# Optimization experiments

Hardware: AMD Instinct MI355X
Metric: run time of the kernel (lower is better)

Reference implementation:

```python
import jax, jax.numpy as jnp
import numpy as np

B, S, H = 2, 2048, 4096
NH, NKV, HD = 32, 8, 128
THETA = 1000000.0
NEG = jnp.finfo(jnp.float32).min


def setup_inputs() -> dict:
    key = jax.random.key(0)
    ks = jax.random.split(key, 9)
    s = 0.02
    return {
        "hidden_states": jax.random.normal(ks[0], (B, S, H), jnp.float32),
        "position_ids": jnp.tile(jnp.arange(S, dtype=jnp.int32)[None, :], (B, 1)),
        "Wq": jax.random.normal(ks[1], (NH * HD, H), jnp.float32) * s,
        "bq": jax.random.normal(ks[2], (NH * HD,), jnp.float32) * s,
        "Wk": jax.random.normal(ks[3], (NKV * HD, H), jnp.float32) * s,
        "bk": jax.random.normal(ks[4], (NKV * HD,), jnp.float32) * s,
        "Wv": jax.random.normal(ks[5], (NKV * HD, H), jnp.float32) * s,
        "bv": jax.random.normal(ks[6], (NKV * HD,), jnp.float32) * s,
        "Wo": jax.random.normal(ks[7], (H, H), jnp.float32) * s,
        "bo": jax.random.normal(ks[8], (H,), jnp.float32) * s,
    }


def _rotate_half_interleaved(x):
    # y[..., ::2] = -x[..., 1::2]; y[..., 1::2] = x[..., ::2]
    x2 = x.reshape(*x.shape[:-1], -1, 2)
    y = jnp.stack([-x2[..., 1], x2[..., 0]], axis=-1)
    return y.reshape(x.shape)


def reference(hidden_states, position_ids, Wq, bq, Wk, bk, Wv, bv, Wo, bo):
    bsz, q_len, _ = hidden_states.shape
    q = (hidden_states @ Wq.T + bq).reshape(bsz, q_len, NH, HD).transpose(0, 2, 1, 3)
    k = (hidden_states @ Wk.T + bk).reshape(bsz, q_len, NKV, HD).transpose(0, 2, 1, 3)
    v = (hidden_states @ Wv.T + bv).reshape(bsz, q_len, NKV, HD).transpose(0, 2, 1, 3)

    # rotary embedding (interleaved / repeat_interleave variant)
    inv_freq = 1.0 / (THETA ** (jnp.arange(0, HD, 2, dtype=jnp.float32) / HD))
    freqs = position_ids.astype(jnp.float32)[:, :, None] * inv_freq[None, None, :]  # [B,S,HD/2]
    emb = jnp.repeat(freqs, 2, axis=-1)  # [B,S,HD]
    cos = jnp.cos(emb)[:, None, :, :]  # [B,1,S,HD]
    sin = jnp.sin(emb)[:, None, :, :]
    q = q * cos + _rotate_half_interleaved(q) * sin
    k = k * cos + _rotate_half_interleaved(k) * sin

    # GQA: repeat KV heads (repeat_interleave on head axis)
    n_rep = NH // NKV
    k = jnp.repeat(k, n_rep, axis=1)
    v = jnp.repeat(v, n_rep, axis=1)

    scores = jnp.einsum("bhqd,bhkd->bhqk", q, k) / np.sqrt(HD).astype(np.float32)
    causal = jnp.tril(jnp.ones((q_len, q_len), dtype=bool))
    scores = jnp.where(causal[None, None, :, :], scores, NEG)
    attn = jax.nn.softmax(scores.astype(jnp.float32), axis=-1).astype(q.dtype)
    out = jnp.einsum("bhqk,bhkd->bhqd", attn, v)
    out = out.transpose(0, 2, 1, 3).reshape(bsz, q_len, H)
    return out @ Wo.T + bo
```

## Files before the change

kernel.cpp:

```cpp
#include <hip/hip_runtime.h>
#include <stdint.h>

typedef __bf16 bf16x8 __attribute__((ext_vector_type(8)));
typedef float f32x4 __attribute__((ext_vector_type(4)));
typedef float f32x16 __attribute__((ext_vector_type(16)));

#define S_LEN 2048
#define NKVH 8
#define HDIM 128
#define MROWS 4096
#define LDQKV 6144
#define SCALE 0.08838834764831845f
#define C_LOG2 0.1275405707067851f
#define THR_RAW 62.7f

__device__ __forceinline__ unsigned short f2bf(float f) {
  unsigned u = __float_as_uint(f);
  u += 0x7FFFu + ((u >> 16) & 1u);
  return (unsigned short)(u >> 16);
}
__device__ __forceinline__ float bf2f(unsigned short h) {
  return __uint_as_float(((unsigned)h) << 16);
}

__device__ __forceinline__ void gload16(const unsigned short* g, unsigned short* l) {
  __builtin_amdgcn_global_load_lds(
      (__attribute__((address_space(1))) void*)(g),
      (__attribute__((address_space(3))) void*)(l), 16, 0, 0);
}

__global__ void cast_f32_bf16(const float4* __restrict__ in, ushort4* __restrict__ out, int n4) {
  int i = blockIdx.x * 256 + threadIdx.x;
  const int stride = gridDim.x * 256;
  for (; i < n4; i += stride) {
    float4 v = in[i];
    ushort4 o;
    o.x = f2bf(v.x); o.y = f2bf(v.y); o.z = f2bf(v.z); o.w = f2bf(v.w);
    out[i] = o;
  }
}

template <int OUTF>
__global__ __launch_bounds__(512, 2)
void gemm256(const unsigned short* __restrict__ A,
             const unsigned short* __restrict__ Bw,
             const float* __restrict__ bias,
             void* __restrict__ C,
             int ldc, int K) {
  __shared__ unsigned short lds[2][4][8192];

  const int t = threadIdx.x;
  const int lane = t & 63;
  const int w = t >> 6;
  const int wr = w >> 2, wc = w & 3;
  const int row16 = lane & 15, kgrp = lane >> 4;
  const int m0 = blockIdx.y * 256, n0 = blockIdx.x * 256;

  const int riu = t >> 3;
  const int col = (((t & 7) ^ (riu & 7)) << 3);
  const int rB0 = (riu & 31) + ((riu >> 5) << 6);
  const unsigned short* pA = A + (size_t)(m0 + riu) * K + col;
  const unsigned short* pB = Bw + (size_t)(n0 + rB0) * K + col;

#define STG(nb_, u_, src_)                                                  \
  {                                                                         \
    gload16((src_), &lds[nb_][u_][t * 8]);                                  \
    gload16((src_) + (size_t)128 * K, &lds[nb_][u_][4096 + t * 8]);         \
  }

  const int sw = row16 & 7;
  const int abase = (wr * 64 + row16) * 64;
  const int bbase = (wc * 32 + row16) * 64;

  f32x4 acc[8][4];
#pragma unroll
  for (int i = 0; i < 8; i++)
#pragma unroll
    for (int j = 0; j < 4; j++) acc[i][j] = (f32x4){0.f, 0.f, 0.f, 0.f};

  bf16x8 afr[4][2], bfr[2][2][2];
  const int NT = K >> 6;

  STG(0, 0, pA);
  STG(0, 1, pB);
  STG(0, 2, pB + (size_t)32 * K);
  STG(0, 3, pA + (size_t)64 * K);

  for (int T = 0; T < NT; ++T) {
    const int cb = T & 1, nb = cb ^ 1;
    const unsigned short* Lc = &lds[cb][0][0];
    const size_t kk = (size_t)(T + 1) << 6;
    const bool st = (T + 1 < NT);

    asm volatile("s_waitcnt vmcnt(4)\n\ts_barrier" ::: "memory");
    if (st) STG(nb, 0, pA + kk);
#pragma unroll
    for (int mi = 0; mi < 4; mi++)
#pragma unroll
      for (int ks = 0; ks < 2; ks++)
        afr[mi][ks] = *(const bf16x8*)(Lc + abase + mi * 1024 + ((((ks << 2) + kgrp) ^ sw) << 3));
#pragma unroll
    for (int nj = 0; nj < 2; nj++)
#pragma unroll
      for (int ks = 0; ks < 2; ks++)
        bfr[0][nj][ks] = *(const bf16x8*)(Lc + 8192 + bbase + nj * 1024 + ((((ks << 2) + kgrp) ^ sw) << 3));
    __builtin_amdgcn_s_setprio(1);
#pragma unroll
    for (int mi = 0; mi < 4; mi++)
#pragma unroll
      for (int nj = 0; nj < 2; nj++)
#pragma unroll
        for (int ks = 0; ks < 2; ks++)
          acc[mi][nj] = __builtin_amdgcn_mfma_f32_16x16x32_bf16(afr[mi][ks], bfr[0][nj][ks], acc[mi][nj], 0, 0, 0);
    __builtin_amdgcn_s_setprio(0);

    if (st) {
      asm volatile("s_waitcnt vmcnt(4)\n\ts_barrier" ::: "memory");
      STG(nb, 1, pB + kk);
    } else {
      asm volatile("s_waitcnt vmcnt(2)\n\ts_barrier" ::: "memory");
    }
#pragma unroll
    for (int nj = 0; nj < 2; nj++)
#pragma unroll
      for (int ks = 0; ks < 2; ks++)
        bfr[1][nj][ks] = *(const bf16x8*)(Lc + 16384 + bbase + nj * 1024 + ((((ks << 2) + kgrp) ^ sw) << 3));
    __builtin_amdgcn_s_setprio(1);
#pragma unroll
    for (int mi = 0; mi < 4; mi++)
#pragma unroll
      for (int nj = 0; nj < 2; nj++)
#pragma unroll
        for (int ks = 0; ks < 2; ks++)
          acc[mi][2 + nj] = __builtin_amdgcn_mfma_f32_16x16x32_bf16(afr[mi][ks], bfr[1][nj][ks], acc[mi][2 + nj], 0, 0, 0);
    __builtin_amdgcn_s_setprio(0);

    if (st) {
      asm volatile("s_waitcnt vmcnt(4)\n\ts_barrier" ::: "memory");
      STG(nb, 2, pB + (size_t)32 * K + kk);
    } else {
      asm volatile("s_waitcnt vmcnt(0)\n\ts_barrier" ::: "memory");
    }
#pragma unroll
    for (int mi = 0; mi < 4; mi++)
#pragma unroll
      for (int ks = 0; ks < 2; ks++)
        afr[mi][ks] = *(const bf16x8*)(Lc + 24576 + abase + mi * 1024 + ((((ks << 2) + kgrp) ^ sw) << 3));
    __builtin_amdgcn_s_setprio(1);
#pragma unroll
    for (int mi = 0; mi < 4; mi++)
#pragma unroll
      for (int nj = 0; nj < 2; nj++)
#pragma unroll
        for (int ks = 0; ks < 2; ks++)
          acc[4 + mi][2 + nj] = __builtin_amdgcn_mfma_f32_16x16x32_bf16(afr[mi][ks], bfr[1][nj][ks], acc[4 + mi][2 + nj], 0, 0, 0);
    __builtin_amdgcn_s_setprio(0);

    if (st) {
      asm volatile("s_waitcnt vmcnt(4)\n\ts_barrier" ::: "memory");
      STG(nb, 3, pA + (size_t)64 * K + kk);
    } else {
      asm volatile("s_barrier" ::: "memory");
    }
    __builtin_amdgcn_s_setprio(1);
#pragma unroll
    for (int mi = 0; mi < 4; mi++)
#pragma unroll
      for (int nj = 0; nj < 2; nj++)
#pragma unroll
        for (int ks = 0; ks < 2; ks++)
          acc[4 + mi][nj] = __builtin_amdgcn_mfma_f32_16x16x32_bf16(afr[mi][ks], bfr[0][nj][ks], acc[4 + mi][nj], 0, 0, 0);
    __builtin_amdgcn_s_setprio(0);
  }
#undef STG

#pragma unroll
  for (int MI = 0; MI < 8; MI++) {
#pragma unroll
    for (int NJ = 0; NJ < 4; NJ++) {
      const int gr = m0 + wr * 128 + MI * 16 + kgrp * 4;
      const int gc = n0 + wc * 64 + NJ * 16 + row16;
      const float bv = bias[gc];
#pragma unroll
      for (int jj = 0; jj < 4; jj++) {
        float v = acc[MI][NJ][jj] + bv;
        if (OUTF) ((float*)C)[(size_t)(gr + jj) * ldc + gc] = v;
        else ((unsigned short*)C)[(size_t)(gr + jj) * ldc + gc] = f2bf(v);
      }
    }
  }
}

template <int OUTF>
__global__ __launch_bounds__(512, 2)
void gemm128(const unsigned short* __restrict__ A,
             const unsigned short* __restrict__ Bw,
             const float* __restrict__ bias,
             void* __restrict__ C,
             int ldc, int K) {
  __shared__ unsigned short lds[3 * 24576];

  const int t = threadIdx.x;
  const int lane = t & 63;
  const int w = t >> 6;
  const int wr = w >> 2, wc = w & 3;
  const int row16 = lane & 15, kgrp = lane >> 4;
  const int m0 = blockIdx.y * 128, n0 = blockIdx.x * 256;

  const int riu = t >> 3;
  const int col = (((t & 7) ^ (riu & 7)) << 3);
  const unsigned short* pA = A + (size_t)(m0 + riu) * K + col;
  const unsigned short* pB = Bw + (size_t)(n0 + riu) * K + col;

#define STG6(bo_, kk_)                                                      \
  {                                                                         \
    gload16(pA + (kk_), &lds[(bo_) + t * 8]);                               \
    gload16(pA + (size_t)64 * K + (kk_), &lds[(bo_) + 4096 + t * 8]);       \
    gload16(pB + (kk_), &lds[(bo_) + 8192 + t * 8]);                        \
    gload16(pB + (size_t)64 * K + (kk_), &lds[(bo_) + 12288 + t * 8]);      \
    gload16(pB + (size_t)128 * K + (kk_), &lds[(bo_) + 16384 + t * 8]);     \
    gload16(pB + (size_t)192 * K + (kk_), &lds[(bo_) + 20480 + t * 8]);     \
  }

  const int sw = row16 & 7;
  const int abase = (wr * 64 + row16) * 64;
  const int bbase = 8192 + (wc * 64 + row16) * 64;

  f32x4 acc[4][4];
#pragma unroll
  for (int i = 0; i < 4; i++)
#pragma unroll
    for (int j = 0; j < 4; j++) acc[i][j] = (f32x4){0.f, 0.f, 0.f, 0.f};

  bf16x8 afr[4][2], bfr[4][2];
  const int NT = K >> 6;

  STG6(0, 0);
  STG6(24576, 64);

  int rbc = 0;
  int rbs = 2;
  for (int T = 0; T < NT; ++T) {
    if (T < NT - 1) { asm volatile("s_waitcnt vmcnt(6)\n\ts_barrier" ::: "memory"); }
    else            { asm volatile("s_waitcnt vmcnt(0)\n\ts_barrier" ::: "memory"); }
    if (T + 2 < NT) STG6(rbs * 24576, (size_t)(T + 2) << 6);
    const unsigned short* Lc = &lds[rbc * 24576];

#pragma unroll
    for (int mi = 0; mi < 4; mi++)
#pragma unroll
      for (int ks = 0; ks < 2; ks++)
        afr[mi][ks] = *(const bf16x8*)(Lc + abase + mi * 1024 + ((((ks << 2) + kgrp) ^ sw) << 3));
#pragma unroll
    for (int nj = 0; nj < 4; nj++)
#pragma unroll
      for (int ks = 0; ks < 2; ks++)
        bfr[nj][ks] = *(const bf16x8*)(Lc + bbase + nj * 1024 + ((((ks << 2) + kgrp) ^ sw) << 3));

    __builtin_amdgcn_s_setprio(1);
#pragma unroll
    for (int mi = 0; mi < 4; mi++)
#pragma unroll
      for (int nj = 0; nj < 4; nj++)
#pragma unroll
        for (int ks = 0; ks < 2; ks++)
          acc[mi][nj] = __builtin_amdgcn_mfma_f32_16x16x32_bf16(afr[mi][ks], bfr[nj][ks], acc[mi][nj], 0, 0, 0);
    __builtin_amdgcn_s_setprio(0);

    rbc++; if (rbc == 3) rbc = 0;
    rbs++; if (rbs == 3) rbs = 0;
  }
#undef STG6

#pragma unroll
  for (int MI = 0; MI < 4; MI++) {
#pragma unroll
    for (int NJ = 0; NJ < 4; NJ++) {
      const int gr = m0 + wr * 64 + MI * 16 + kgrp * 4;
      const int gc = n0 + wc * 64 + NJ * 16 + row16;
      const float bv = bias[gc];
#pragma unroll
      for (int jj = 0; jj < 4; jj++) {
        float v = acc[MI][NJ][jj] + bv;
        if (OUTF) ((float*)C)[(size_t)(gr + jj) * ldc + gc] = v;
        else ((unsigned short*)C)[(size_t)(gr + jj) * ldc + gc] = f2bf(v);
      }
    }
  }
}

__global__ void rope_kernel(unsigned short* __restrict__ X,
                            const int* __restrict__ pos_ids,
                            int ncols, int ld) {
  const int perrow = ncols >> 3;
  int idx = blockIdx.x * 256 + threadIdx.x;
  const int row = idx / perrow;
  const int c0 = (idx - row * perrow) << 3;
  const float pos = (float)pos_ids[row];
  unsigned short* p = X + (size_t)row * ld + c0;
  uint4 v = *(uint4*)p;
  unsigned short* e = (unsigned short*)&v;
  const int p0 = (c0 & 127) >> 1;
#pragma unroll
  for (int q = 0; q < 4; ++q) {
    const float inv = exp2f(-(float)(p0 + q) * (19.931568569324174f / 64.f));
    const float fr = pos * inv;
    float sn, cs;
    __sincosf(fr, &sn, &cs);
    const float xe = bf2f(e[2 * q]);
    const float xo = bf2f(e[2 * q + 1]);
    e[2 * q]     = f2bf(xe * cs - xo * sn);
    e[2 * q + 1] = f2bf(xo * cs + xe * sn);
  }
  *(uint4*)p = v;
}

__global__ void transpose_v(const unsigned short* __restrict__ V, int ldv,
                            unsigned short* __restrict__ Vt) {
  __shared__ unsigned short tile[32][40];
  const int t = threadIdx.x;
  const int n0 = blockIdx.x * 32;
  const int m0 = blockIdx.y * 32;
  const int r = t >> 3;
  const int c = (t & 7) << 2;
  const unsigned short* src = V + (size_t)(m0 + r) * ldv + n0 + c;
  ushort4 d = *(const ushort4*)src;
  tile[r][c] = d.x; tile[r][c + 1] = d.y; tile[r][c + 2] = d.z; tile[r][c + 3] = d.w;
  __syncthreads();
  const int b = m0 >> 11;
  unsigned short* dst = Vt + (size_t)(b * 1024 + n0 + r) * 2048 + (m0 & 2047) + c;
  ushort4 o;
  o.x = tile[c][r]; o.y = tile[c + 1][r]; o.z = tile[c + 2][r]; o.w = tile[c + 3][r];
  *(ushort4*)dst = o;
}

__global__ __launch_bounds__(512, 2)
void attn_kernel2(const unsigned short* __restrict__ QKV,
                  const unsigned short* __restrict__ Vt,
                  unsigned short* __restrict__ O) {
  __shared__ unsigned short sK[2][64 * 128];
  __shared__ unsigned short sV[2][128 * 64];

  const int t = threadIdx.x;
  const int lane = t & 63;
  const int w = t >> 6;
  const int l31 = lane & 31;
  const int hi = lane >> 5;
  const int bid = blockIdx.x;
  int qt, bh;
  if (bid < 256) { qt = 7 - (bid >> 6); bh = bid & 63; }
  else           { qt = (bid - 256) >> 6; bh = bid & 63; }
  const int b = bh >> 5, h = bh & 31;
  const int kh = h >> 2;
  const int q0 = qt * 256;
  const int qw = q0 + w * 32;
  const int qg = qw + l31;

  const int ntiles = (q0 + 256) >> 6;
  const int myTiles = (qw + 95) >> 6;

  const int krow0 = t >> 4;
  const int kslot = t & 15;
  const int vrow0 = t >> 3;
  const int vslot = t & 7;
  const unsigned short* Kp = QKV + (size_t)(b * S_LEN) * LDQKV + 4096 + kh * HDIM;
  const unsigned short* Vp = Vt + (size_t)(b * 1024 + kh * HDIM) * 2048;
  const int ksw = (kslot ^ (krow0 & 7)) << 3;
  const int vsw = (vslot ^ (vrow0 & 7)) << 3;
  const unsigned short* KpA = Kp + (size_t)krow0 * LDQKV + ksw;
  const unsigned short* KpB = Kp + (size_t)(krow0 + 32) * LDQKV + ksw;
  const unsigned short* VpA = Vp + (size_t)vrow0 * 2048 + vsw;
  const unsigned short* VpB = Vp + (size_t)(vrow0 + 64) * 2048 + vsw;

#define STAGE(bufi, kv0m)                                              \
  {                                                                    \
    gload16(KpA + (size_t)(kv0m)*LDQKV, &sK[bufi][t * 8]);             \
    gload16(KpB + (size_t)(kv0m)*LDQKV, &sK[bufi][4096 + t * 8]);      \
    gload16(VpA + (kv0m), &sV[bufi][t * 8]);                           \
    gload16(VpB + (kv0m), &sV[bufi][4096 + t * 8]);                    \
  }

  bf16x8 qf[8];
  {
    const unsigned short* qb = QKV + (size_t)(b * S_LEN + qw + l31) * LDQKV + h * HDIM + hi * 8;
#pragma unroll
    for (int kd = 0; kd < 8; kd++) qf[kd] = *(const bf16x8*)(qb + kd * 16);
  }

  f32x16 o[4];
#pragma unroll
  for (int nt = 0; nt < 4; nt++)
#pragma unroll
    for (int r = 0; r < 16; r++) o[nt][r] = 0.f;
  float m = -1e30f, lsum = 0.f;

  const int rw7 = (l31 & 7) << 4;
  const int kswz = (hi << 4) ^ rw7;
  const int kbase0 = l31 * 128;
  const int vbase = l31 * 64;

  STAGE(0, 0);
  int buf = 0;
  for (int it = 0; it < ntiles; ++it) {
    if (it + 1 < ntiles) {
      STAGE(buf ^ 1, (it + 1) << 6);
      asm volatile("s_waitcnt vmcnt(4)" ::: "memory");
    } else {
      asm volatile("s_waitcnt vmcnt(0)" ::: "memory");
    }
    __builtin_amdgcn_s_barrier();

    if (it < myTiles) {
      const unsigned short* sKc = &sK[buf][0];
      const unsigned short* sVc = &sV[buf][0];
      const int kv0 = it << 6;

      f32x16 st[2];
#pragma unroll
      for (int r = 0; r < 16; r++) { st[0][r] = 0.f; st[1][r] = 0.f; }
      __builtin_amdgcn_s_setprio(1);
#pragma unroll
      for (int kd = 0; kd < 8; kd++) {
        bf16x8 k0 = *(const bf16x8*)(sKc + kbase0 + (((kd << 5) ^ kswz) >> 1));
        bf16x8 k1 = *(const bf16x8*)(sKc + 4096 + kbase0 + (((kd << 5) ^ kswz) >> 1));
        st[0] = __builtin_amdgcn_mfma_f32_32x32x16_bf16(k0, qf[kd], st[0], 0, 0, 0);
        st[1] = __builtin_amdgcn_mfma_f32_32x32x16_bf16(k1, qf[kd], st[1], 0, 0, 0);
      }
      __builtin_amdgcn_s_setprio(0);

      if (it == myTiles - 1) {
#pragma unroll
        for (int s2 = 0; s2 < 2; s2++)
#pragma unroll
          for (int r = 0; r < 16; r++) {
            const int kvg = kv0 + s2 * 32 + (r & 3) + 8 * (r >> 2) + 4 * hi;
            if (kvg > qg) st[s2][r] = -1e30f;
          }
      }

      float mx[8];
#pragma unroll
      for (int r = 0; r < 8; r++)
        mx[r] = fmaxf(fmaxf(st[0][r], st[0][r + 8]), fmaxf(st[1][r], st[1][r + 8]));
#pragma unroll
      for (int d = 4; d >= 1; d >>= 1)
#pragma unroll
        for (int r = 0; r < d; r++) mx[r] = fmaxf(mx[r], mx[r + d]);
      float tmax = fmaxf(mx[0], __shfl_xor(mx[0], 32));

      if (!__all(tmax <= m + THR_RAW)) {
        const float mnew = fmaxf(m, tmax);
        const float corr = exp2f((m - mnew) * C_LOG2);
        lsum *= corr;
#pragma unroll
        for (int r = 0; r < 16; r++) {
          const int src = (r & 3) + 8 * (r >> 2) + 4 * hi;
          const float cr = __shfl(corr, src);
#pragma unroll
          for (int nt = 0; nt < 4; nt++) o[nt][r] *= cr;
        }
        m = mnew;
      }
      const float mC = m * C_LOG2;

#pragma unroll
      for (int s2 = 0; s2 < 2; s2++)
#pragma unroll
        for (int r = 0; r < 16; r++) st[s2][r] = exp2f(fmaf(st[s2][r], C_LOG2, -mC));
      float sm[8];
#pragma unroll
      for (int r = 0; r < 8; r++)
        sm[r] = (st[0][r] + st[0][r + 8]) + (st[1][r] + st[1][r + 8]);
#pragma unroll
      for (int d = 4; d >= 1; d >>= 1)
#pragma unroll
        for (int r = 0; r < d; r++) sm[r] += sm[r + d];
      float tsum = sm[0] + __shfl_xor(sm[0], 32);
      lsum += tsum;

      bf16x8 pa[4];
#pragma unroll
      for (int s2 = 0; s2 < 2; s2++) {
        unsigned pw[8];
#pragma unroll
        for (int i = 0; i < 8; i++)
          asm("v_cvt_pk_bf16_f32 %0, %1, %2" : "=v"(pw[i]) : "v"(st[s2][2 * i]), "v"(st[s2][2 * i + 1]));
        const unsigned x0 = (unsigned)__shfl_xor((int)pw[0], 32);
        const unsigned x1 = (unsigned)__shfl_xor((int)pw[1], 32);
        const unsigned x2 = (unsigned)__shfl_xor((int)pw[2], 32);
        const unsigned x3 = (unsigned)__shfl_xor((int)pw[3], 32);
        const unsigned x4 = (unsigned)__shfl_xor((int)pw[4], 32);
        const unsigned x5 = (unsigned)__shfl_xor((int)pw[5], 32);
        const unsigned x6 = (unsigned)__shfl_xor((int)pw[6], 32);
        const unsigned x7 = (unsigned)__shfl_xor((int)pw[7], 32);
        union { unsigned u[4]; bf16x8 v; } u0, u1;
        u0.u[0] = hi ? x2 : pw[0];
        u0.u[1] = hi ? x3 : pw[1];
        u0.u[2] = hi ? pw[2] : x0;
        u0.u[3] = hi ? pw[3] : x1;
        u1.u[0] = hi ? x6 : pw[4];
        u1.u[1] = hi ? x7 : pw[5];
        u1.u[2] = hi ? pw[6] : x4;
        u1.u[3] = hi ? pw[7] : x5;
        pa[2 * s2] = u0.v; pa[2 * s2 + 1] = u1.v;
      }

      __builtin_amdgcn_s_setprio(1);
#pragma unroll
      for (int nt = 0; nt < 4; nt++) {
        const unsigned short* vr = sVc + vbase + nt * 2048;
#pragma unroll
        for (int ks = 0; ks < 4; ks++) {
          bf16x8 vb = *(const bf16x8*)(vr + (((ks << 5) ^ kswz) >> 1));
          o[nt] = __builtin_amdgcn_mfma_f32_32x32x16_bf16(pa[ks], vb, o[nt], 0, 0, 0);
        }
      }
      __builtin_amdgcn_s_setprio(0);
    }

    asm volatile("" ::: "memory");
    __builtin_amdgcn_s_barrier();
    buf ^= 1;
  }

  const float linv = 1.0f / lsum;
#pragma unroll
  for (int r = 0; r < 16; r++) {
    const int qr = (r & 3) + 8 * (r >> 2) + 4 * hi;
    const float lr = __shfl(linv, qr);
    unsigned short* orow = O + (size_t)(b * S_LEN + qw + qr) * 4096 + h * HDIM + l31;
#pragma unroll
    for (int nt = 0; nt < 4; nt++) orow[nt * 32] = f2bf(o[nt][r] * lr);
  }
#undef STAGE
}

extern "C" void kernel_launch(void* const* d_in, const int* in_sizes, int n_in,
                              void* d_out, int out_size, void* d_ws, size_t ws_size,
                              hipStream_t stream) {
  const float* hs = (const float*)d_in[0];
  const int*  pos = (const int*)d_in[1];
  const float* Wq = (const float*)d_in[2];
  const float* bq = (const float*)d_in[3];
  const float* Wk = (const float*)d_in[4];
  const float* bk = (const float*)d_in[5];
  const float* Wv = (const float*)d_in[6];
  const float* bv = (const float*)d_in[7];
  const float* Wo = (const float*)d_in[8];
  const float* bo = (const float*)d_in[9];
  float* out = (float*)d_out;

  char* ws = (char*)d_ws;
  unsigned short* hbf  = (unsigned short*)(ws);
  unsigned short* Wbuf = (unsigned short*)(ws + 33554432);
  unsigned short* QKV  = (unsigned short*)(ws + 83886080);
  unsigned short* Vtb  = (unsigned short*)(ws + 134217728);
  float*          biasb= (float*)(ws + 142606336);

  cast_f32_bf16<<<2048, 256, 0, stream>>>((const float4*)hs, (ushort4*)hbf, 4194304);
  cast_f32_bf16<<<2048, 256, 0, stream>>>((const float4*)Wq, (ushort4*)Wbuf, 4194304);
  cast_f32_bf16<<<1024, 256, 0, stream>>>((const float4*)Wk, (ushort4*)(Wbuf + 16777216), 1048576);
  cast_f32_bf16<<<1024, 256, 0, stream>>>((const float4*)Wv, (ushort4*)(Wbuf + 20971520), 1048576);
  hipMemcpyAsync(biasb, bq, 4096 * 4, hipMemcpyDeviceToDevice, stream);
  hipMemcpyAsync(biasb + 4096, bk, 1024 * 4, hipMemcpyDeviceToDevice, stream);
  hipMemcpyAsync(biasb + 5120, bv, 1024 * 4, hipMemcpyDeviceToDevice, stream);

  gemm256<0><<<dim3(16, 16), 512, 0, stream>>>(hbf, Wbuf, biasb, QKV, LDQKV, 4096);
  gemm128<0><<<dim3(8, 32), 512, 0, stream>>>(hbf, Wbuf + 16777216, biasb + 4096, QKV + 4096, LDQKV, 4096);

  cast_f32_bf16<<<2048, 256, 0, stream>>>((const float4*)Wo, (ushort4*)Wbuf, 4194304);

  rope_kernel<<<8192, 256, 0, stream>>>(QKV, pos, 4096, LDQKV);
  rope_kernel<<<2048, 256, 0, stream>>>(QKV + 4096, pos, 1024, LDQKV);

  transpose_v<<<dim3(32, 128), 256, 0, stream>>>(QKV + 5120, LDQKV, Vtb);

  attn_kernel2<<<dim3(512), 512, 0, stream>>>(QKV, Vtb, hbf);

  gemm256<1><<<dim3(16, 16), 512, 0, stream>>>(hbf, Wbuf, bo, out, 4096, 4096);
}
```

Baseline: 528.8 us.

## Shrink attention blocks to 128 queries, single-buffer KV, raise occupancy

The attention kernel now uses 256-thread blocks covering 128 query rows instead of 512 threads covering 256, and launches twice as many blocks. K/V staging drops from double-buffered to single-buffered shared memory, which halves LDS per block so about four blocks fit per CU. The block-to-query-tile order is reshuffled to interleave heavy and light causal tiles. The cost is that loads are no longer overlapped with compute within a block, so latency hiding relies on the other resident blocks, and each K/V tile is now loaded by more blocks.

```diff
diff --git a/kernel.cpp b/kernel.cpp
--- a/kernel.cpp
+++ b/kernel.cpp
@@ -334,12 +334,12 @@
   *(ushort4*)dst = o;
 }
 
-__global__ __launch_bounds__(512, 2)
-void attn_kernel2(const unsigned short* __restrict__ QKV,
+__global__ __launch_bounds__(256, 4)
+void attn_kernel3(const unsigned short* __restrict__ QKV,
                   const unsigned short* __restrict__ Vt,
                   unsigned short* __restrict__ O) {
-  __shared__ unsigned short sK[2][64 * 128];
-  __shared__ unsigned short sV[2][128 * 64];
+  __shared__ unsigned short sK[64 * 128];
+  __shared__ unsigned short sV[128 * 64];
 
   const int t = threadIdx.x;
   const int lane = t & 63;
@@ -347,16 +347,15 @@
   const int l31 = lane & 31;
   const int hi = lane >> 5;
   const int bid = blockIdx.x;
-  int qt, bh;
-  if (bid < 256) { qt = 7 - (bid >> 6); bh = bid & 63; }
-  else           { qt = (bid - 256) >> 6; bh = bid & 63; }
+  const int g = bid >> 6, bh = bid & 63;
+  const int qt = (g < 4) ? (15 - g) : (g < 8) ? (g - 4) : (g < 12) ? (19 - g) : (g - 8);
   const int b = bh >> 5, h = bh & 31;
   const int kh = h >> 2;
-  const int q0 = qt * 256;
+  const int q0 = qt << 7;
   const int qw = q0 + w * 32;
   const int qg = qw + l31;
 
-  const int ntiles = (q0 + 256) >> 6;
+  const int ntiles = (q0 + 128) >> 6;
   const int myTiles = (qw + 95) >> 6;
 
   const int krow0 = t >> 4;
@@ -368,16 +367,16 @@
   const int ksw = (kslot ^ (krow0 & 7)) << 3;
   const int vsw = (vslot ^ (vrow0 & 7)) << 3;
   const unsigned short* KpA = Kp + (size_t)krow0 * LDQKV + ksw;
-  const unsigned short* KpB = Kp + (size_t)(krow0 + 32) * LDQKV + ksw;
   const unsigned short* VpA = Vp + (size_t)vrow0 * 2048 + vsw;
-  const unsigned short* VpB = Vp + (size_t)(vrow0 + 64) * 2048 + vsw;
-
-#define STAGE(bufi, kv0m)                                              \
-  {                                                                    \
-    gload16(KpA + (size_t)(kv0m)*LDQKV, &sK[bufi][t * 8]);             \
-    gload16(KpB + (size_t)(kv0m)*LDQKV, &sK[bufi][4096 + t * 8]);      \
-    gload16(VpA + (kv0m), &sV[bufi][t * 8]);                           \
-    gload16(VpB + (kv0m), &sV[bufi][4096 + t * 8]);                    \
+
+#define STAGE(kv0m)                                                         \
+  {                                                                         \
+    _Pragma("unroll")                                                       \
+    for (int p = 0; p < 4; p++)                                             \
+      gload16(KpA + (size_t)((kv0m) + 16 * p) * LDQKV, &sK[p * 2048 + t * 8]); \
+    _Pragma("unroll")                                                       \
+    for (int p = 0; p < 4; p++)                                             \
+      gload16(VpA + (kv0m) + p * 65536, &sV[p * 2048 + t * 8]);             \
   }
 
   bf16x8 qf[8];
@@ -399,20 +398,12 @@
   const int kbase0 = l31 * 128;
   const int vbase = l31 * 64;
 
-  STAGE(0, 0);
-  int buf = 0;
   for (int it = 0; it < ntiles; ++it) {
-    if (it + 1 < ntiles) {
-      STAGE(buf ^ 1, (it + 1) << 6);
-      asm volatile("s_waitcnt vmcnt(4)" ::: "memory");
-    } else {
-      asm volatile("s_waitcnt vmcnt(0)" ::: "memory");
-    }
+    STAGE(it << 6);
+    asm volatile("s_waitcnt vmcnt(0)" ::: "memory");
     __builtin_amdgcn_s_barrier();
 
     if (it < myTiles) {
-      const unsigned short* sKc = &sK[buf][0];
-      const unsigned short* sVc = &sV[buf][0];
       const int kv0 = it << 6;
 
       f32x16 st[2];
@@ -421,8 +412,8 @@
       __builtin_amdgcn_s_setprio(1);
 #pragma unroll
       for (int kd = 0; kd < 8; kd++) {
-        bf16x8 k0 = *(const bf16x8*)(sKc + kbase0 + (((kd << 5) ^ kswz) >> 1));
-        bf16x8 k1 = *(const bf16x8*)(sKc + 4096 + kbase0 + (((kd << 5) ^ kswz) >> 1));
+        bf16x8 k0 = *(const bf16x8*)(sK + kbase0 + (((kd << 5) ^ kswz) >> 1));
+        bf16x8 k1 = *(const bf16x8*)(sK + 4096 + kbase0 + (((kd << 5) ^ kswz) >> 1));
         st[0] = __builtin_amdgcn_mfma_f32_32x32x16_bf16(k0, qf[kd], st[0], 0, 0, 0);
         st[1] = __builtin_amdgcn_mfma_f32_32x32x16_bf16(k1, qf[kd], st[1], 0, 0, 0);
       }
@@ -508,7 +499,7 @@
       __builtin_amdgcn_s_setprio(1);
 #pragma unroll
       for (int nt = 0; nt < 4; nt++) {
-        const unsigned short* vr = sVc + vbase + nt * 2048;
+        const unsigned short* vr = sV + vbase + nt * 2048;
 #pragma unroll
         for (int ks = 0; ks < 4; ks++) {
           bf16x8 vb = *(const bf16x8*)(vr + (((ks << 5) ^ kswz) >> 1));
@@ -518,9 +509,7 @@
       __builtin_amdgcn_s_setprio(0);
     }
 
-    asm volatile("" ::: "memory");
     __builtin_amdgcn_s_barrier();
-    buf ^= 1;
   }
 
   const float linv = 1.0f / lsum;
@@ -575,7 +564,7 @@
 
   transpose_v<<<dim3(32, 128), 256, 0, stream>>>(QKV + 5120, LDQKV, Vtb);
 
-  attn_kernel2<<<dim3(512), 512, 0, stream>>>(QKV, Vtb, hbf);
+  attn_kernel3<<<dim3(1024), 256, 0, stream>>>(QKV, Vtb, hbf);
 
   gemm256<1><<<dim3(16, 16), 512, 0, stream>>>(hbf, Wbuf, bo, out, 4096, 4096);
 }
```

Result: slower. 796.4 us (+50.6%).
